# Optimization experiments

Hardware: AMD Instinct MI355X
Metric: run time of the kernel (lower is better)

## Reference

```python
import jax, jax.numpy as jnp
import numpy as np

B, T, N, H, L = 64, 256, 512, 1024, 2


def setup_inputs() -> dict:
    key = jax.random.key(0)
    ks = jax.random.split(key, 12)
    s = 0.02  # weight init scale
    return {
        "x": jax.random.normal(ks[0], (B, T, N), jnp.float32),
        "h": jax.random.normal(ks[1], (L, B, H), jnp.float32),
        "c": jax.random.normal(ks[2], (L, B, H), jnp.float32),
        # layer 0: input dim N
        "W_ih0": jax.random.normal(ks[3], (4 * H, N), jnp.float32) * s,
        "W_hh0": jax.random.normal(ks[4], (4 * H, H), jnp.float32) * s,
        "b_ih0": jax.random.normal(ks[5], (4 * H,), jnp.float32) * s,
        "b_hh0": jax.random.normal(ks[6], (4 * H,), jnp.float32) * s,
        # layer 1: input dim H
        "W_ih1": jax.random.normal(ks[7], (4 * H, H), jnp.float32) * s,
        "W_hh1": jax.random.normal(ks[8], (4 * H, H), jnp.float32) * s,
        "b_ih1": jax.random.normal(ks[9], (4 * H,), jnp.float32) * s,
        "b_hh1": jax.random.normal(ks[10], (4 * H,), jnp.float32) * s,
    }


def _lstm_cell(x_t, h_l, c_l, Wi, Wh, bi, bh):
    # gates: [B, 4H], torch LSTMCell gate order i, f, g, o
    gates = x_t @ Wi.T + h_l @ Wh.T + bi + bh
    i, f, g, o = jnp.split(gates, 4, axis=-1)
    i, f, o = jax.nn.sigmoid(i), jax.nn.sigmoid(f), jax.nn.sigmoid(o)
    g = jnp.tanh(g)
    c_new = f * c_l + i * g
    h_new = o * jnp.tanh(c_new)
    return h_new, c_new


def reference(x, h, c, W_ih0, W_hh0, b_ih0, b_hh0, W_ih1, W_hh1, b_ih1, b_hh1):
    params = [(W_ih0, W_hh0, b_ih0, b_hh0), (W_ih1, W_hh1, b_ih1, b_hh1)]

    def step(carry, x_t):
        h, c = carry  # each [L, B, H]
        inp = x_t
        new_h, new_c = [], []
        for l, (Wi, Wh, bi, bh) in enumerate(params):
            h_new, c_new = _lstm_cell(inp, h[l], c[l], Wi, Wh, bi, bh)
            new_h.append(h_new)
            new_c.append(c_new)
            inp = h_new
        return (jnp.stack(new_h), jnp.stack(new_c)), inp

    xT = jnp.swapaxes(x, 0, 1)  # [T, B, N]
    (h_final, c_final), outsT = jax.lax.scan(step, (h, c), xT)
    outs = jnp.swapaxes(outsT, 0, 1)  # [B, T, H]
    return outs, h_final, c_final
```

## Files before the change

kernel.cpp:

```cpp
#include <hip/hip_runtime.h>
#include <hip/hip_bf16.h>


#define T_ 256
#define B_ 64
#define N_ 512
#define H_ 1024
#define FH_ 4096
#define NWG_SEQ 256
#define BH_ (B_ * H_)

typedef _Float16 f16;
typedef _Float16 f16x4 __attribute__((ext_vector_type(4)));
typedef _Float16 f16x8 __attribute__((ext_vector_type(8)));
typedef float f32x4 __attribute__((ext_vector_type(4)));
typedef unsigned long long ull;

template <bool V> struct BC { static constexpr bool value = V; };

__device__ __forceinline__ float sigf(float x) { return 1.f / (1.f + __expf(-x)); }
__device__ __forceinline__ float tanhf_fast(float x) { return 1.f - 2.f / (__expf(2.f * x) + 1.f); }

__device__ __forceinline__ void st_u64g(ull* p, ull v) {
  __hip_atomic_store(p, v, __ATOMIC_RELAXED, __HIP_MEMORY_SCOPE_AGENT);
}
__device__ __forceinline__ void st_u32g(unsigned* p, unsigned v) {
  __hip_atomic_store(p, v, __ATOMIC_RELAXED, __HIP_MEMORY_SCOPE_AGENT);
}
__device__ __forceinline__ ull ld_u64g(const ull* p) {
  return __hip_atomic_load(p, __ATOMIC_RELAXED, __HIP_MEMORY_SCOPE_AGENT);
}
__device__ __forceinline__ f16x8 ld_b128_nc(const f16* p) {
  f16x8 r;
  asm volatile("global_load_dwordx4 %0, %1, off sc0 sc1" : "=v"(r) : "v"(p));
  return r;
}

__global__ __launch_bounds__(256) void init_all(
    const float* __restrict__ x, const float* __restrict__ h,
    const float* __restrict__ Wih0, const float* __restrict__ bih0, const float* __restrict__ bhh0,
    const float* __restrict__ Whh0, const float* __restrict__ Wih1, const float* __restrict__ Whh1,
    const float* __restrict__ bih1, const float* __restrict__ bhh1,
    f16* __restrict__ xT, f16* __restrict__ wih0, f16* __restrict__ whh0,
    f16* __restrict__ wih1, f16* __restrict__ whh1,
    float* __restrict__ bias0, float* __restrict__ bias1,
    f16* __restrict__ hinit, unsigned* __restrict__ flags)
{
  const int stride = gridDim.x * blockDim.x;
  const int t0 = blockIdx.x * blockDim.x + threadIdx.x;

  for (int i = t0; i < T_ * B_ * N_; i += stride) {
    int n = i & (N_ - 1);
    int tb = i >> 9;
    int b = tb & (B_ - 1);
    int t = tb >> 6;
    xT[i] = (f16)x[((size_t)b * T_ + t) * N_ + n];
  }
  for (int i = t0; i < FH_ * N_; i += stride) wih0[i] = (f16)Wih0[i];
  for (int i = t0; i < FH_ * H_; i += stride) {
    whh0[i] = (f16)Whh0[i];
    wih1[i] = (f16)Wih1[i];
    whh1[i] = (f16)Whh1[i];
  }
  for (int i = t0; i < FH_; i += stride) {
    bias0[i] = bih0[i] + bhh0[i];
    bias1[i] = bih1[i] + bhh1[i];
  }
  for (int i = t0; i < 2 * BH_; i += stride) hinit[i] = (f16)h[i];
  if (t0 < 512) flags[t0] = 0u;
}

__global__ __launch_bounds__(256) void gemm_pre0(
    const f16* __restrict__ xT, const f16* __restrict__ wih0,
    const float* __restrict__ bias0, f16* __restrict__ pre0T)
{
  const int wid = threadIdx.x >> 6;
  const int lane = threadIdx.x & 63;
  const int lr = lane & 15;
  const int lkq = (lane >> 4) << 3;
  const int lrq = (lane >> 4) << 2;

  const int mt = blockIdx.x & 255;
  const int ct = (blockIdx.x >> 8) * 4 + wid;
  const int row0 = mt * 64, col0 = ct * 64;

  f32x4 acc[4][4] = {};
  const f16* Abase = xT + (size_t)row0 * N_;

  #pragma unroll 2
  for (int kk = 0; kk < N_ / 32; ++kk) {
    const int k = kk * 32 + lkq;
    f16x8 a[4], b[4];
    #pragma unroll
    for (int r = 0; r < 4; ++r)
      a[r] = *(const f16x8*)(Abase + (size_t)(r * 16 + lr) * N_ + k);
    #pragma unroll
    for (int cf = 0; cf < 4; ++cf)
      b[cf] = *(const f16x8*)(wih0 + (size_t)(col0 + cf * 16 + lr) * N_ + k);
    #pragma unroll
    for (int r = 0; r < 4; ++r)
      #pragma unroll
      for (int cf = 0; cf < 4; ++cf)
        acc[r][cf] = __builtin_amdgcn_mfma_f32_16x16x32_f16(a[r], b[cf], acc[r][cf], 0, 0, 0);
  }

  #pragma unroll
  for (int r = 0; r < 4; ++r) {
    #pragma unroll
    for (int cf = 0; cf < 4; ++cf) {
      const int col = col0 + cf * 16 + lr;
      const float bv = bias0[col];
      f16x4 pv;
      #pragma unroll
      for (int ri = 0; ri < 4; ++ri) pv[ri] = (f16)(acc[r][cf][ri] + bv);
      *(f16x4*)(pre0T + ((size_t)mt * FH_ + col) * 64 + r * 16 + lrq) = pv;
    }
  }
}

template <bool DEEP>
__global__ __launch_bounds__(256, 1) void lstm_seq(
    const f16* __restrict__ pre0T, const f16* __restrict__ whh0,
    const f16* __restrict__ wih1, const f16* __restrict__ whh1,
    const float* __restrict__ bias1, const f16* __restrict__ hinit,
    const float* __restrict__ cin,
    f16* __restrict__ h0r, f16* __restrict__ h1r,
    float* __restrict__ out, unsigned* __restrict__ flags)
{
  __shared__ __align__(16) float exc[2][4][32][33];
  __shared__ __align__(16) f16 smH[2][32][8];

  const int tid = threadIdx.x;
  const int p = tid >> 6;
  const int lane = tid & 63;
  const int lr = lane & 15;
  const int lq = lane >> 4;
  const int lkq = lq << 3;
  const int lrq = lq << 2;

  const int wg = blockIdx.x;
  const int pod = wg >> 7;
  const int slot = wg & 127;
  const int rs = pod << 5;
  const int ub = slot << 3;
  unsigned* f0p = flags + (pod << 7);
  unsigned* f1p = flags + 256 + (pod << 7);

  auto rt = [&](int t) -> size_t { return DEEP ? (size_t)t : (size_t)(t & 7); };

  f16x8 l0w[2][8], l1aw[2][8], l1bw[2][8];
  #pragma unroll
  for (int cf = 0; cf < 2; ++cf) {
    const size_t wr = (size_t)((2 * cf + (lr >> 3)) * H_ + ub + (lr & 7)) * H_;
    #pragma unroll
    for (int j = 0; j < 8; ++j) {
      const int k = (p * 8 + j) * 32 + lkq;
      l0w[cf][j]  = *(const f16x8*)(whh0 + wr + k);
      l1aw[cf][j] = *(const f16x8*)(wih1 + wr + k);
      l1bw[cf][j] = *(const f16x8*)(whh1 + wr + k);
    }
  }

  const int crow = tid & 31;
  const int cu = tid >> 5;
  const size_t cell = (size_t)(rs + crow) * H_ + ub + cu;
  float c0 = cin[cell];
  float c1 = cin[(size_t)BH_ + cell];
  float b1v[4];
  #pragma unroll
  for (int g = 0; g < 4; ++g) b1v[g] = bias1[g * H_ + ub + cu];

  float* outh = out + (size_t)B_ * T_ * H_;
  float* outc = outh + 2 * BH_;

  auto waitwide = [&](const unsigned* base, unsigned tgt) {
    const ull* fp = (const ull*)base;
    for (;;) {
      ull v = ld_u64g(&fp[lane]);
      const bool ok = ((unsigned)v >= tgt) && ((unsigned)(v >> 32) >= tgt);
      if (__ballot(ok) == ~0ull) break;
      __builtin_amdgcn_s_sleep(1);
    }
    asm volatile("" ::: "memory");
  };

  auto body = [&](auto A0c, auto A1c, int e) {
    constexpr bool A0 = decltype(A0c)::value;
    constexpr bool A1 = decltype(A1c)::value;

    float pf[4];
    if (A0) {
      #pragma unroll
      for (int g = 0; g < 4; ++g)
        pf[g] = (float)pre0T[((size_t)e * FH_ + g * H_ + ub + cu) * 64 + rs + crow];
    }

    if (p == 0) {
      if (!DEEP && e >= 7) waitwide(f1p, (unsigned)(e - 6));
      if (e > 0) waitwide(f0p, (unsigned)e);
    }
    __syncthreads();

    const f16* h0s = ((e == 0) ? hinit : h0r + rt(e - 1) * BH_) + (size_t)rs * H_;
    f16x8 a0v[8], a1v[8];
    #pragma unroll
    for (int j = 0; j < 8; ++j) {
      const int k = (p * 8 + j) * 32 + lkq;
      if constexpr (DEEP) {
        a0v[j] = *(const f16x8*)(h0s + (size_t)lr * H_ + k);
        a1v[j] = *(const f16x8*)(h0s + (size_t)(16 + lr) * H_ + k);
      } else {
        a0v[j] = ld_b128_nc(h0s + (size_t)lr * H_ + k);
        a1v[j] = ld_b128_nc(h0s + (size_t)(16 + lr) * H_ + k);
      }
    }
    if (!DEEP) {
      asm volatile("s_waitcnt vmcnt(0)" ::: "memory");
      __builtin_amdgcn_sched_barrier(0);
    }

    float hn0 = 0.f, cn0 = 0.f;
    if (A0) {
      f32x4 acc0[2][2] = {};
      #pragma unroll
      for (int j = 0; j < 8; ++j)
        #pragma unroll
        for (int cf = 0; cf < 2; ++cf) {
          acc0[cf][0] = __builtin_amdgcn_mfma_f32_16x16x32_f16(a0v[j], l0w[cf][j], acc0[cf][0], 0, 0, 0);
          acc0[cf][1] = __builtin_amdgcn_mfma_f32_16x16x32_f16(a1v[j], l0w[cf][j], acc0[cf][1], 0, 0, 0);
        }
      #pragma unroll
      for (int cf = 0; cf < 2; ++cf)
        #pragma unroll
        for (int rf = 0; rf < 2; ++rf)
          #pragma unroll
          for (int ri = 0; ri < 4; ++ri)
            exc[0][p][rf * 16 + lrq + ri][cf * 16 + lr] = acc0[cf][rf][ri];
    }
    __syncthreads();

    if (A0) {
      float gv[4];
      #pragma unroll
      for (int g = 0; g < 4; ++g)
        gv[g] = exc[0][0][crow][g * 8 + cu] + exc[0][1][crow][g * 8 + cu]
              + exc[0][2][crow][g * 8 + cu] + exc[0][3][crow][g * 8 + cu] + pf[g];
      cn0 = sigf(gv[1]) * c0 + sigf(gv[0]) * tanhf_fast(gv[2]);
      hn0 = sigf(gv[3]) * tanhf_fast(cn0);
      c0 = cn0;
      smH[0][crow][cu] = (f16)hn0;
    }
    __syncthreads();

    if (A0 && p == 0) {
      const int row = lane >> 1, half = lane & 1;
      ull v = *(const ull*)&smH[0][row][half * 4];
      st_u64g((ull*)(h0r + rt(e) * BH_ + (size_t)(rs + row) * H_ + ub + half * 4), v);
      asm volatile("s_waitcnt vmcnt(0)" ::: "memory");
      if (lane == 0) st_u32g(&f0p[slot], (unsigned)(e + 1));
    }

    float hn1 = 0.f, cn1 = 0.f;
    if (A1) {
      if (p == 0 && e >= 2) waitwide(f1p, (unsigned)e);
      __syncthreads();

      const f16* h1s = ((e == 1) ? hinit + BH_ : h1r + rt(e - 2) * BH_) + (size_t)rs * H_;
      f16x8 c0v[8], c1v[8];
      #pragma unroll
      for (int j = 0; j < 8; ++j) {
        const int k = (p * 8 + j) * 32 + lkq;
        if constexpr (DEEP) {
          c0v[j] = *(const f16x8*)(h1s + (size_t)lr * H_ + k);
          c1v[j] = *(const f16x8*)(h1s + (size_t)(16 + lr) * H_ + k);
        } else {
          c0v[j] = ld_b128_nc(h1s + (size_t)lr * H_ + k);
          c1v[j] = ld_b128_nc(h1s + (size_t)(16 + lr) * H_ + k);
        }
      }

      f32x4 acc1[2][2] = {};
      #pragma unroll
      for (int j = 0; j < 8; ++j)
        #pragma unroll
        for (int cf = 0; cf < 2; ++cf) {
          acc1[cf][0] = __builtin_amdgcn_mfma_f32_16x16x32_f16(a0v[j], l1aw[cf][j], acc1[cf][0], 0, 0, 0);
          acc1[cf][1] = __builtin_amdgcn_mfma_f32_16x16x32_f16(a1v[j], l1aw[cf][j], acc1[cf][1], 0, 0, 0);
        }
      if (!DEEP) {
        asm volatile("s_waitcnt vmcnt(0)" ::: "memory");
        __builtin_amdgcn_sched_barrier(0);
      }
      #pragma unroll
      for (int j = 0; j < 8; ++j)
        #pragma unroll
        for (int cf = 0; cf < 2; ++cf) {
          acc1[cf][0] = __builtin_amdgcn_mfma_f32_16x16x32_f16(c0v[j], l1bw[cf][j], acc1[cf][0], 0, 0, 0);
          acc1[cf][1] = __builtin_amdgcn_mfma_f32_16x16x32_f16(c1v[j], l1bw[cf][j], acc1[cf][1], 0, 0, 0);
        }

      #pragma unroll
      for (int cf = 0; cf < 2; ++cf)
        #pragma unroll
        for (int rf = 0; rf < 2; ++rf)
          #pragma unroll
          for (int ri = 0; ri < 4; ++ri)
            exc[1][p][rf * 16 + lrq + ri][cf * 16 + lr] = acc1[cf][rf][ri];
      __syncthreads();

      float gv[4];
      #pragma unroll
      for (int g = 0; g < 4; ++g)
        gv[g] = exc[1][0][crow][g * 8 + cu] + exc[1][1][crow][g * 8 + cu]
              + exc[1][2][crow][g * 8 + cu] + exc[1][3][crow][g * 8 + cu] + b1v[g];
      cn1 = sigf(gv[1]) * c1 + sigf(gv[0]) * tanhf_fast(gv[2]);
      hn1 = sigf(gv[3]) * tanhf_fast(cn1);
      c1 = cn1;
      smH[1][crow][cu] = (f16)hn1;
      __syncthreads();

      if (p == 1) {
        const int row = lane >> 1, half = lane & 1;
        ull v = *(const ull*)&smH[1][row][half * 4];
        st_u64g((ull*)(h1r + rt(e - 1) * BH_ + (size_t)(rs + row) * H_ + ub + half * 4), v);
        asm volatile("s_waitcnt vmcnt(0)" ::: "memory");
        if (lane == 0) st_u32g(&f1p[slot], (unsigned)(e + 1));
      }
    }

    if (A0 && e == T_ - 1) { outh[cell] = hn0; outc[cell] = cn0; }
    if (A1) {
      out[(size_t)(rs + crow) * (T_ * H_) + (size_t)(e - 1) * H_ + ub + cu] = hn1;
      if (e == T_) { outh[BH_ + cell] = hn1; outc[BH_ + cell] = cn1; }
    }
  };

  body(BC<true>{}, BC<false>{}, 0);
  for (int e = 1; e < T_; ++e) body(BC<true>{}, BC<true>{}, e);
  body(BC<false>{}, BC<true>{}, T_);
}

extern "C" void kernel_launch(void* const* d_in, const int* in_sizes, int n_in,
                              void* d_out, int out_size, void* d_ws, size_t ws_size,
                              hipStream_t stream)
{
  const float* x    = (const float*)d_in[0];
  const float* h    = (const float*)d_in[1];
  const float* c    = (const float*)d_in[2];
  const float* Wih0 = (const float*)d_in[3];
  const float* Whh0 = (const float*)d_in[4];
  const float* bih0 = (const float*)d_in[5];
  const float* bhh0 = (const float*)d_in[6];
  const float* Wih1 = (const float*)d_in[7];
  const float* Whh1 = (const float*)d_in[8];
  const float* bih1 = (const float*)d_in[9];
  const float* bhh1 = (const float*)d_in[10];

  char* w = (char*)d_ws;
  size_t off = 0;
  auto carve = [&](size_t bytes) -> char* {
    char* ptr = w + off;
    off = (off + bytes + 255) & ~(size_t)255;
    return ptr;
  };
  f16*   pre0T = (f16*)  carve((size_t)T_ * B_ * FH_ * 2);
  f16*   xT    = (f16*)  carve((size_t)T_ * B_ * N_ * 2);
  f16*   wih0  = (f16*)  carve((size_t)FH_ * N_ * 2);
  f16*   whh0  = (f16*)  carve((size_t)FH_ * H_ * 2);
  f16*   wih1  = (f16*)  carve((size_t)FH_ * H_ * 2);
  f16*   whh1  = (f16*)  carve((size_t)FH_ * H_ * 2);
  float* bias0 = (float*)carve((size_t)FH_ * 4);
  float* bias1 = (float*)carve((size_t)FH_ * 4);
  f16*   hinit = (f16*)  carve((size_t)2 * BH_ * 2);
  f16*   h0s   = (f16*)  carve((size_t)8 * BH_ * 2);
  f16*   h1s   = (f16*)  carve((size_t)8 * BH_ * 2);
  unsigned* flags = (unsigned*)carve(512 * 4);
  const size_t base_end = off;
  f16*   h0ring = (f16*) carve((size_t)T_ * BH_ * 2);
  f16*   h1ring = (f16*) carve((size_t)T_ * BH_ * 2);
  const bool deep = (off <= ws_size);
  if (base_end > ws_size) return;

  init_all<<<2048, 256, 0, stream>>>(x, h, Wih0, bih0, bhh0, Whh0, Wih1, Whh1, bih1, bhh1,
                                     xT, wih0, whh0, wih1, whh1, bias0, bias1, hinit, flags);
  gemm_pre0<<<4096, 256, 0, stream>>>(xT, wih0, bias0, pre0T);
  if (deep)
    lstm_seq<true><<<NWG_SEQ, 256, 0, stream>>>(pre0T, whh0, wih1, whh1, bias1, hinit,
                                                (const float*)c, h0ring, h1ring,
                                                (float*)d_out, flags);
  else
    lstm_seq<false><<<NWG_SEQ, 256, 0, stream>>>(pre0T, whh0, wih1, whh1, bias1, hinit,
                                                 (const float*)c, h0s, h1s,
                                                 (float*)d_out, flags);
}
```

Before: 1.944 ms.

## Split layer 0 and layer 1 into separate warp groups running concurrently

The sequential LSTM kernel now launches 512 threads per workgroup. One 256-thread group runs the layer-0 recurrence and the other runs layer 1, each with its own weight registers and cell state. The groups synchronise internally through an LDS atomic counter instead of __syncthreads, and layer 1 waits on layer 0's global flags per step. This lets the two layers pipeline independently rather than in one interleaved body, which should shorten the per-step critical path. The cost is more registers and waves per CU, plus spin-based intra-group barriers.

```diff
diff --git a/kernel.cpp b/kernel.cpp
--- a/kernel.cpp
+++ b/kernel.cpp
@@ -15,8 +15,6 @@
 typedef _Float16 f16x8 __attribute__((ext_vector_type(8)));
 typedef float f32x4 __attribute__((ext_vector_type(4)));
 typedef unsigned long long ull;
-
-template <bool V> struct BC { static constexpr bool value = V; };
 
 __device__ __forceinline__ float sigf(float x) { return 1.f / (1.f + __expf(-x)); }
 __device__ __forceinline__ float tanhf_fast(float x) { return 1.f - 2.f / (__expf(2.f * x) + 1.f); }
@@ -67,7 +65,7 @@
     bias1[i] = bih1[i] + bhh1[i];
   }
   for (int i = t0; i < 2 * BH_; i += stride) hinit[i] = (f16)h[i];
-  if (t0 < 512) flags[t0] = 0u;
+  if (t0 < 1024) flags[t0] = 0u;
 }
 
 __global__ __launch_bounds__(256) void gemm_pre0(
@@ -119,7 +117,7 @@
 }
 
 template <bool DEEP>
-__global__ __launch_bounds__(256, 1) void lstm_seq(
+__global__ __launch_bounds__(512, 1) void lstm_seq(
     const f16* __restrict__ pre0T, const f16* __restrict__ whh0,
     const f16* __restrict__ wih1, const f16* __restrict__ whh1,
     const float* __restrict__ bias1, const f16* __restrict__ hinit,
@@ -129,9 +127,12 @@
 {
   __shared__ __align__(16) float exc[2][4][32][33];
   __shared__ __align__(16) f16 smH[2][32][8];
+  __shared__ unsigned gbar[2];
 
   const int tid = threadIdx.x;
-  const int p = tid >> 6;
+  const int g = tid >> 8;
+  const int gtid = tid & 255;
+  const int p = gtid >> 6;
   const int lane = tid & 63;
   const int lr = lane & 15;
   const int lq = lane >> 4;
@@ -146,32 +147,21 @@
   unsigned* f0p = flags + (pod << 7);
   unsigned* f1p = flags + 256 + (pod << 7);
 
+  if (tid < 2) gbar[tid] = 0u;
+  __syncthreads();
+
   auto rt = [&](int t) -> size_t { return DEEP ? (size_t)t : (size_t)(t & 7); };
 
-  f16x8 l0w[2][8], l1aw[2][8], l1bw[2][8];
-  #pragma unroll
-  for (int cf = 0; cf < 2; ++cf) {
-    const size_t wr = (size_t)((2 * cf + (lr >> 3)) * H_ + ub + (lr & 7)) * H_;
-    #pragma unroll
-    for (int j = 0; j < 8; ++j) {
-      const int k = (p * 8 + j) * 32 + lkq;
-      l0w[cf][j]  = *(const f16x8*)(whh0 + wr + k);
-      l1aw[cf][j] = *(const f16x8*)(wih1 + wr + k);
-      l1bw[cf][j] = *(const f16x8*)(whh1 + wr + k);
-    }
-  }
-
-  const int crow = tid & 31;
-  const int cu = tid >> 5;
-  const size_t cell = (size_t)(rs + crow) * H_ + ub + cu;
-  float c0 = cin[cell];
-  float c1 = cin[(size_t)BH_ + cell];
-  float b1v[4];
-  #pragma unroll
-  for (int g = 0; g < 4; ++g) b1v[g] = bias1[g * H_ + ub + cu];
-
-  float* outh = out + (size_t)B_ * T_ * H_;
-  float* outc = outh + 2 * BH_;
+  unsigned bt = 0;
+  auto groupbar = [&]() {
+    asm volatile("s_waitcnt lgkmcnt(0)" ::: "memory");
+    bt += 4;
+    if (lane == 0)
+      __hip_atomic_fetch_add(&gbar[g], 1u, __ATOMIC_RELAXED, __HIP_MEMORY_SCOPE_WORKGROUP);
+    while (__hip_atomic_load(&gbar[g], __ATOMIC_RELAXED, __HIP_MEMORY_SCOPE_WORKGROUP) < bt)
+      __builtin_amdgcn_s_sleep(1);
+    asm volatile("" ::: "memory");
+  };
 
   auto waitwide = [&](const unsigned* base, unsigned tgt) {
     const ull* fp = (const ull*)base;
@@ -184,50 +174,58 @@
     asm volatile("" ::: "memory");
   };
 
-  auto body = [&](auto A0c, auto A1c, int e) {
-    constexpr bool A0 = decltype(A0c)::value;
-    constexpr bool A1 = decltype(A1c)::value;
-
-    float pf[4];
-    if (A0) {
-      #pragma unroll
-      for (int g = 0; g < 4; ++g)
-        pf[g] = (float)pre0T[((size_t)e * FH_ + g * H_ + ub + cu) * 64 + rs + crow];
-    }
-
-    if (p == 0) {
-      if (!DEEP && e >= 7) waitwide(f1p, (unsigned)(e - 6));
+  const int crow = gtid & 31;
+  const int cu = gtid >> 5;
+  const size_t cell = (size_t)(rs + crow) * H_ + ub + cu;
+  float cst = cin[(size_t)g * BH_ + cell];
+
+  float* outh = out + (size_t)B_ * T_ * H_;
+  float* outc = outh + 2 * BH_;
+
+  if (g == 0) {
+    f16x8 l0w[2][8];
+    #pragma unroll
+    for (int cf = 0; cf < 2; ++cf) {
+      const size_t wr = (size_t)((2 * cf + (lr >> 3)) * H_ + ub + (lr & 7)) * H_;
+      #pragma unroll
+      for (int j = 0; j < 8; ++j)
+        l0w[cf][j] = *(const f16x8*)(whh0 + wr + (p * 8 + j) * 32 + lkq);
+    }
+
+    for (int e = 0; e < T_; ++e) {
+      float pf[4];
+      #pragma unroll
+      for (int gg = 0; gg < 4; ++gg)
+        pf[gg] = (float)pre0T[((size_t)e * FH_ + gg * H_ + ub + cu) * 64 + rs + crow];
+
       if (e > 0) waitwide(f0p, (unsigned)e);
-    }
-    __syncthreads();
-
-    const f16* h0s = ((e == 0) ? hinit : h0r + rt(e - 1) * BH_) + (size_t)rs * H_;
-    f16x8 a0v[8], a1v[8];
-    #pragma unroll
-    for (int j = 0; j < 8; ++j) {
-      const int k = (p * 8 + j) * 32 + lkq;
-      if constexpr (DEEP) {
-        a0v[j] = *(const f16x8*)(h0s + (size_t)lr * H_ + k);
-        a1v[j] = *(const f16x8*)(h0s + (size_t)(16 + lr) * H_ + k);
-      } else {
-        a0v[j] = ld_b128_nc(h0s + (size_t)lr * H_ + k);
-        a1v[j] = ld_b128_nc(h0s + (size_t)(16 + lr) * H_ + k);
-      }
-    }
-    if (!DEEP) {
-      asm volatile("s_waitcnt vmcnt(0)" ::: "memory");
-      __builtin_amdgcn_sched_barrier(0);
-    }
-
-    float hn0 = 0.f, cn0 = 0.f;
-    if (A0) {
-      f32x4 acc0[2][2] = {};
+      if (!DEEP && e >= 8) waitwide(f1p, (unsigned)(e - 7));
+
+      const f16* h0s = ((e == 0) ? hinit : h0r + rt(e - 1) * BH_) + (size_t)rs * H_;
+      f16x8 a0v[8], a1v[8];
+      #pragma unroll
+      for (int j = 0; j < 8; ++j) {
+        const int k = (p * 8 + j) * 32 + lkq;
+        if constexpr (DEEP) {
+          a0v[j] = *(const f16x8*)(h0s + (size_t)lr * H_ + k);
+          a1v[j] = *(const f16x8*)(h0s + (size_t)(16 + lr) * H_ + k);
+        } else {
+          a0v[j] = ld_b128_nc(h0s + (size_t)lr * H_ + k);
+          a1v[j] = ld_b128_nc(h0s + (size_t)(16 + lr) * H_ + k);
+        }
+      }
+      if (!DEEP) {
+        asm volatile("s_waitcnt vmcnt(0)" ::: "memory");
+        __builtin_amdgcn_sched_barrier(0);
+      }
+
+      f32x4 acc[2][2] = {};
       #pragma unroll
       for (int j = 0; j < 8; ++j)
         #pragma unroll
         for (int cf = 0; cf < 2; ++cf) {
-          acc0[cf][0] = __builtin_amdgcn_mfma_f32_16x16x32_f16(a0v[j], l0w[cf][j], acc0[cf][0], 0, 0, 0);
-          acc0[cf][1] = __builtin_amdgcn_mfma_f32_16x16x32_f16(a1v[j], l0w[cf][j], acc0[cf][1], 0, 0, 0);
+          acc[cf][0] = __builtin_amdgcn_mfma_f32_16x16x32_f16(a0v[j], l0w[cf][j], acc[cf][0], 0, 0, 0);
+          acc[cf][1] = __builtin_amdgcn_mfma_f32_16x16x32_f16(a1v[j], l0w[cf][j], acc[cf][1], 0, 0, 0);
         }
       #pragma unroll
       for (int cf = 0; cf < 2; ++cf)
@@ -235,58 +233,89 @@
         for (int rf = 0; rf < 2; ++rf)
           #pragma unroll
           for (int ri = 0; ri < 4; ++ri)
-            exc[0][p][rf * 16 + lrq + ri][cf * 16 + lr] = acc0[cf][rf][ri];
-    }
-    __syncthreads();
-
-    if (A0) {
+            exc[0][p][rf * 16 + lrq + ri][cf * 16 + lr] = acc[cf][rf][ri];
+      groupbar();
+
       float gv[4];
       #pragma unroll
-      for (int g = 0; g < 4; ++g)
-        gv[g] = exc[0][0][crow][g * 8 + cu] + exc[0][1][crow][g * 8 + cu]
-              + exc[0][2][crow][g * 8 + cu] + exc[0][3][crow][g * 8 + cu] + pf[g];
-      cn0 = sigf(gv[1]) * c0 + sigf(gv[0]) * tanhf_fast(gv[2]);
-      hn0 = sigf(gv[3]) * tanhf_fast(cn0);
-      c0 = cn0;
-      smH[0][crow][cu] = (f16)hn0;
-    }
-    __syncthreads();
-
-    if (A0 && p == 0) {
-      const int row = lane >> 1, half = lane & 1;
-      ull v = *(const ull*)&smH[0][row][half * 4];
-      st_u64g((ull*)(h0r + rt(e) * BH_ + (size_t)(rs + row) * H_ + ub + half * 4), v);
-      asm volatile("s_waitcnt vmcnt(0)" ::: "memory");
-      if (lane == 0) st_u32g(&f0p[slot], (unsigned)(e + 1));
-    }
-
-    float hn1 = 0.f, cn1 = 0.f;
-    if (A1) {
-      if (p == 0 && e >= 2) waitwide(f1p, (unsigned)e);
-      __syncthreads();
-
-      const f16* h1s = ((e == 1) ? hinit + BH_ : h1r + rt(e - 2) * BH_) + (size_t)rs * H_;
-      f16x8 c0v[8], c1v[8];
+      for (int gg = 0; gg < 4; ++gg)
+        gv[gg] = exc[0][0][crow][gg * 8 + cu] + exc[0][1][crow][gg * 8 + cu]
+               + exc[0][2][crow][gg * 8 + cu] + exc[0][3][crow][gg * 8 + cu] + pf[gg];
+      const float cn = sigf(gv[1]) * cst + sigf(gv[0]) * tanhf_fast(gv[2]);
+      const float hn = sigf(gv[3]) * tanhf_fast(cn);
+      cst = cn;
+      smH[0][crow][cu] = (f16)hn;
+      groupbar();
+
+      if (p == 0) {
+        const int row = lane >> 1, half = lane & 1;
+        ull v = *(const ull*)&smH[0][row][half * 4];
+        st_u64g((ull*)(h0r + rt(e) * BH_ + (size_t)(rs + row) * H_ + ub + half * 4), v);
+        asm volatile("s_waitcnt vmcnt(0)" ::: "memory");
+        if (lane == 0) st_u32g(&f0p[slot], (unsigned)(e + 1));
+      }
+
+      if (e == T_ - 1) { outh[cell] = hn; outc[cell] = cn; }
+    }
+  } else {
+    f16x8 l1aw[2][8], l1bw[2][8];
+    #pragma unroll
+    for (int cf = 0; cf < 2; ++cf) {
+      const size_t wr = (size_t)((2 * cf + (lr >> 3)) * H_ + ub + (lr & 7)) * H_;
+      #pragma unroll
+      for (int j = 0; j < 8; ++j) {
+        const int k = (p * 8 + j) * 32 + lkq;
+        l1aw[cf][j] = *(const f16x8*)(wih1 + wr + k);
+        l1bw[cf][j] = *(const f16x8*)(whh1 + wr + k);
+      }
+    }
+    float b1v[4];
+    #pragma unroll
+    for (int gg = 0; gg < 4; ++gg) b1v[gg] = bias1[gg * H_ + ub + cu];
+
+    for (int t = 0; t < T_; ++t) {
+      waitwide(f0p, (unsigned)(t + 1));
+      const f16* h0s = h0r + rt(t) * BH_ + (size_t)rs * H_;
+      f16x8 a0v[8], a1v[8];
       #pragma unroll
       for (int j = 0; j < 8; ++j) {
         const int k = (p * 8 + j) * 32 + lkq;
         if constexpr (DEEP) {
-          c0v[j] = *(const f16x8*)(h1s + (size_t)lr * H_ + k);
-          c1v[j] = *(const f16x8*)(h1s + (size_t)(16 + lr) * H_ + k);
+          a0v[j] = *(const f16x8*)(h0s + (size_t)lr * H_ + k);
+          a1v[j] = *(const f16x8*)(h0s + (size_t)(16 + lr) * H_ + k);
         } else {
-          c0v[j] = ld_b128_nc(h1s + (size_t)lr * H_ + k);
-          c1v[j] = ld_b128_nc(h1s + (size_t)(16 + lr) * H_ + k);
-        }
-      }
-
-      f32x4 acc1[2][2] = {};
+          a0v[j] = ld_b128_nc(h0s + (size_t)lr * H_ + k);
+          a1v[j] = ld_b128_nc(h0s + (size_t)(16 + lr) * H_ + k);
+        }
+      }
+      if (!DEEP) {
+        asm volatile("s_waitcnt vmcnt(0)" ::: "memory");
+        __builtin_amdgcn_sched_barrier(0);
+      }
+
+      f32x4 acc[2][2] = {};
       #pragma unroll
       for (int j = 0; j < 8; ++j)
         #pragma unroll
         for (int cf = 0; cf < 2; ++cf) {
-          acc1[cf][0] = __builtin_amdgcn_mfma_f32_16x16x32_f16(a0v[j], l1aw[cf][j], acc1[cf][0], 0, 0, 0);
-          acc1[cf][1] = __builtin_amdgcn_mfma_f32_16x16x32_f16(a1v[j], l1aw[cf][j], acc1[cf][1], 0, 0, 0);
-        }
+          acc[cf][0] = __builtin_amdgcn_mfma_f32_16x16x32_f16(a0v[j], l1aw[cf][j], acc[cf][0], 0, 0, 0);
+          acc[cf][1] = __builtin_amdgcn_mfma_f32_16x16x32_f16(a1v[j], l1aw[cf][j], acc[cf][1], 0, 0, 0);
+        }
+
+      if (t > 0) waitwide(f1p, (unsigned)t);
+      const f16* h1s = ((t == 0) ? hinit + BH_ : h1r + rt(t - 1) * BH_) + (size_t)rs * H_;
+      f16x8 d0v[8], d1v[8];
+      #pragma unroll
+      for (int j = 0; j < 8; ++j) {
+        const int k = (p * 8 + j) * 32 + lkq;
+        if constexpr (DEEP) {
+          d0v[j] = *(const f16x8*)(h1s + (size_t)lr * H_ + k);
+          d1v[j] = *(const f16x8*)(h1s + (size_t)(16 + lr) * H_ + k);
+        } else {
+          d0v[j] = ld_b128_nc(h1s + (size_t)lr * H_ + k);
+          d1v[j] = ld_b128_nc(h1s + (size_t)(16 + lr) * H_ + k);
+        }
+      }
       if (!DEEP) {
         asm volatile("s_waitcnt vmcnt(0)" ::: "memory");
         __builtin_amdgcn_sched_barrier(0);
@@ -295,8 +324,8 @@
       for (int j = 0; j < 8; ++j)
         #pragma unroll
         for (int cf = 0; cf < 2; ++cf) {
-          acc1[cf][0] = __builtin_amdgcn_mfma_f32_16x16x32_f16(c0v[j], l1bw[cf][j], acc1[cf][0], 0, 0, 0);
-          acc1[cf][1] = __builtin_amdgcn_mfma_f32_16x16x32_f16(c1v[j], l1bw[cf][j], acc1[cf][1], 0, 0, 0);
+          acc[cf][0] = __builtin_amdgcn_mfma_f32_16x16x32_f16(d0v[j], l1bw[cf][j], acc[cf][0], 0, 0, 0);
+          acc[cf][1] = __builtin_amdgcn_mfma_f32_16x16x32_f16(d1v[j], l1bw[cf][j], acc[cf][1], 0, 0, 0);
         }
 
       #pragma unroll
@@ -305,39 +334,32 @@
         for (int rf = 0; rf < 2; ++rf)
           #pragma unroll
           for (int ri = 0; ri < 4; ++ri)
-            exc[1][p][rf * 16 + lrq + ri][cf * 16 + lr] = acc1[cf][rf][ri];
-      __syncthreads();
+            exc[1][p][rf * 16 + lrq + ri][cf * 16 + lr] = acc[cf][rf][ri];
+      groupbar();
 
       float gv[4];
       #pragma unroll
-      for (int g = 0; g < 4; ++g)
-        gv[g] = exc[1][0][crow][g * 8 + cu] + exc[1][1][crow][g * 8 + cu]
-              + exc[1][2][crow][g * 8 + cu] + exc[1][3][crow][g * 8 + cu] + b1v[g];
-      cn1 = sigf(gv[1]) * c1 + sigf(gv[0]) * tanhf_fast(gv[2]);
-      hn1 = sigf(gv[3]) * tanhf_fast(cn1);
-      c1 = cn1;
-      smH[1][crow][cu] = (f16)hn1;
-      __syncthreads();
-
-      if (p == 1) {
+      for (int gg = 0; gg < 4; ++gg)
+        gv[gg] = exc[1][0][crow][gg * 8 + cu] + exc[1][1][crow][gg * 8 + cu]
+               + exc[1][2][crow][gg * 8 + cu] + exc[1][3][crow][gg * 8 + cu] + b1v[gg];
+      const float cn = sigf(gv[1]) * cst + sigf(gv[0]) * tanhf_fast(gv[2]);
+      const float hn = sigf(gv[3]) * tanhf_fast(cn);
+      cst = cn;
+      smH[1][crow][cu] = (f16)hn;
+      groupbar();
+
+      if (p == 0) {
         const int row = lane >> 1, half = lane & 1;
         ull v = *(const ull*)&smH[1][row][half * 4];
-        st_u64g((ull*)(h1r + rt(e - 1) * BH_ + (size_t)(rs + row) * H_ + ub + half * 4), v);
+        st_u64g((ull*)(h1r + rt(t) * BH_ + (size_t)(rs + row) * H_ + ub + half * 4), v);
         asm volatile("s_waitcnt vmcnt(0)" ::: "memory");
-        if (lane == 0) st_u32g(&f1p[slot], (unsigned)(e + 1));
-      }
-    }
-
-    if (A0 && e == T_ - 1) { outh[cell] = hn0; outc[cell] = cn0; }
-    if (A1) {
-      out[(size_t)(rs + crow) * (T_ * H_) + (size_t)(e - 1) * H_ + ub + cu] = hn1;
-      if (e == T_) { outh[BH_ + cell] = hn1; outc[BH_ + cell] = cn1; }
-    }
-  };
-
-  body(BC<true>{}, BC<false>{}, 0);
-  for (int e = 1; e < T_; ++e) body(BC<true>{}, BC<true>{}, e);
-  body(BC<false>{}, BC<true>{}, T_);
+        if (lane == 0) st_u32g(&f1p[slot], (unsigned)(t + 1));
+      }
+
+      out[(size_t)(rs + crow) * (T_ * H_) + (size_t)t * H_ + ub + cu] = hn;
+      if (t == T_ - 1) { outh[BH_ + cell] = hn; outc[BH_ + cell] = cn; }
+    }
+  }
 }
 
 extern "C" void kernel_launch(void* const* d_in, const int* in_sizes, int n_in,
@@ -374,7 +396,7 @@
   f16*   hinit = (f16*)  carve((size_t)2 * BH_ * 2);
   f16*   h0s   = (f16*)  carve((size_t)8 * BH_ * 2);
   f16*   h1s   = (f16*)  carve((size_t)8 * BH_ * 2);
-  unsigned* flags = (unsigned*)carve(512 * 4);
+  unsigned* flags = (unsigned*)carve(1024 * 4);
   const size_t base_end = off;
   f16*   h0ring = (f16*) carve((size_t)T_ * BH_ * 2);
   f16*   h1ring = (f16*) carve((size_t)T_ * BH_ * 2);
@@ -385,11 +407,11 @@
                                      xT, wih0, whh0, wih1, whh1, bias0, bias1, hinit, flags);
   gemm_pre0<<<4096, 256, 0, stream>>>(xT, wih0, bias0, pre0T);
   if (deep)
-    lstm_seq<true><<<NWG_SEQ, 256, 0, stream>>>(pre0T, whh0, wih1, whh1, bias1, hinit,
+    lstm_seq<true><<<NWG_SEQ, 512, 0, stream>>>(pre0T, whh0, wih1, whh1, bias1, hinit,
                                                 (const float*)c, h0ring, h1ring,
                                                 (float*)d_out, flags);
   else
-    lstm_seq<false><<<NWG_SEQ, 256, 0, stream>>>(pre0T, whh0, wih1, whh1, bias1, hinit,
+    lstm_seq<false><<<NWG_SEQ, 512, 0, stream>>>(pre0T, whh0, wih1, whh1, bias1, hinit,
                                                  (const float*)c, h0s, h1s,
                                                  (float*)d_out, flags);
 }
```

New measurement: 3.716 ms. +91.1%, slower.
